# Performance work log

Hardware: AMD Instinct MI355X
Metric: run time of the kernel (lower is better)

Reference implementation:

```python
import jax, jax.numpy as jnp
import numpy as np

B, D_CAT, C_IN, C_OUT, K, H, W = 16, 512, 256, 256, 3, 64, 64


def setup_inputs() -> dict:
    key = jax.random.key(0)
    ks = jax.random.split(key, 9)
    inp = {
        "x": jax.random.normal(ks[0], (B, C_IN, H, W), dtype=jnp.float32),
        "y": jax.random.normal(ks[1], (B, D_CAT), dtype=jnp.float32),
        # EqualLinear stack: d_catin -> in_channels, then n_dl=2 layers in_channels -> in_channels
        "w0": jax.random.normal(ks[2], (C_IN, D_CAT), dtype=jnp.float32) / np.sqrt(D_CAT),
        "b0": jnp.zeros((C_IN,), dtype=jnp.float32),
        "w1": jax.random.normal(ks[3], (C_IN, C_IN), dtype=jnp.float32) / np.sqrt(C_IN),
        "b1": jnp.zeros((C_IN,), dtype=jnp.float32),
        "w2": jax.random.normal(ks[4], (C_IN, C_IN), dtype=jnp.float32) / np.sqrt(C_IN),
        "b2": jnp.zeros((C_IN,), dtype=jnp.float32),
        # shared conv weight (O, I, k, k), modulated per sample
        "conv_w": jax.random.normal(ks[5], (C_OUT, C_IN, K, K), dtype=jnp.float32) / np.sqrt(C_IN * K * K),
    }
    return inp


def _lrelu(z):
    # nn.LeakyReLU default negative_slope = 0.01
    return jnp.where(z >= 0, z, 0.01 * z)


def reference(x, y, w0, b0, w1, b1, w2, b2, conv_w):
    # style MLP (EqualLinear stack with LeakyReLU)
    s = _lrelu(y @ w0.T + b0)          # (B, C_in)
    s = _lrelu(s @ w1.T + b1)
    s = _lrelu(s @ w2.T + b2)
    # Per-sample weight modulation: conv(x[b], W * s[b, None, :, None, None]).
    # Since the scale is per input channel (no demodulation), this is exactly
    # equivalent to scaling the input channels and running one shared conv —
    # the fused form a custom kernel would use.
    x_mod = x * s[:, :, None, None]    # (B, C_in, H, W)
    out = jax.lax.conv_general_dilated(
        x_mod, conv_w,
        window_strides=(1, 1),
        padding=((1, 1), (1, 1)),
        dimension_numbers=("NCHW", "OIHW", "NCHW"),
    )  # (B, C_out, H, W); conv has bias=False in _DyConv
    return out
```

## Files before the change

### kernel.cpp

```cpp
#include <hip/hip_runtime.h>

typedef short bf16x8 __attribute__((ext_vector_type(8)));
typedef float f32x4 __attribute__((ext_vector_type(4)));
typedef unsigned short ushort8 __attribute__((ext_vector_type(8)));
typedef unsigned short ushort4v __attribute__((ext_vector_type(4)));

#define BATCH 16
#define DCAT 512
#define CIN 256
#define COUT 256
#define HH 64
#define WW 64
#define HP 66
#define WP 66
#define PLANE (HP * WP * 8)

__device__ __forceinline__ unsigned short f2bf(float f) {
  unsigned int u = __float_as_uint(f);
  unsigned int r = (u + 0x7fffu + ((u >> 16) & 1u)) >> 16;
  return (unsigned short)r;
}

template <int IN_DIM>
__global__ void __launch_bounds__(256) mlp_layer(const float* __restrict__ in,
                                                 const float* __restrict__ w,
                                                 const float* __restrict__ bias,
                                                 float* __restrict__ out) {
  int wid = threadIdx.x >> 6, lane = threadIdx.x & 63;
  int oidx = blockIdx.x * 4 + wid;
  int b = oidx >> 8, c = oidx & 255;
  const float* wr = w + (size_t)c * IN_DIM;
  const float* ir = in + (size_t)b * IN_DIM;
  float sum = 0.f;
#pragma unroll
  for (int d0 = 0; d0 < IN_DIM; d0 += 256) {
    f32x4 wv = *(const f32x4*)(wr + d0 + lane * 4);
    f32x4 iv = *(const f32x4*)(ir + d0 + lane * 4);
    sum += wv[0] * iv[0] + wv[1] * iv[1] + wv[2] * iv[2] + wv[3] * iv[3];
  }
#pragma unroll
  for (int off = 32; off; off >>= 1) sum += __shfl_xor(sum, off, 64);
  if (lane == 0) {
    float a = sum + bias[c];
    out[oidx] = a >= 0.f ? a : 0.01f * a;
  }
}

__global__ void __launch_bounds__(256) prep_all(const float* __restrict__ t1,
                                                const float* __restrict__ w2,
                                                const float* __restrict__ b2,
                                                const float* __restrict__ x,
                                                const float* __restrict__ cw,
                                                unsigned short* __restrict__ xpad,
                                                unsigned short* __restrict__ wt) {
  int blk = blockIdx.x;
  int tid = threadIdx.x;

  if (blk >= 1024) {
    int idx = (blk - 1024) * 256 + tid;
    int t = idx / 16384;
    int r = idx - t * 16384;
    int o = r >> 6, i4 = r & 63;
    ushort4v v;
#pragma unroll
    for (int j = 0; j < 4; j++) v[j] = f2bf(cw[(o * 256 + i4 * 4 + j) * 9 + t]);
    *(ushort4v*)(wt + ((size_t)(t * COUT + o)) * CIN + i4 * 4) = v;
    return;
  }

  int h = blk & 1, c8 = (blk >> 1) & 31, b = blk >> 6;
  int wid = tid >> 6, lane = tid & 63;

  float tv = t1[b * CIN + tid];
  float pj[8];
#pragma unroll
  for (int j = 0; j < 8; j++) pj[j] = w2[(size_t)(c8 * 8 + j) * CIN + tid] * tv;

  const float* xb = x + ((size_t)(b * CIN + c8 * 8)) * (HH * WW);
  int gg0 = h * 512 + tid;
  int gg1 = gg0 + 256;
  int hh0 = (gg0 >> 4) + 1, w00 = (gg0 & 15) * 4 + 1;
  int hh1 = (gg1 >> 4) + 1, w01 = (gg1 & 15) * 4 + 1;
  int base0 = (hh0 - 1) * WW + (w00 - 1);
  int base1 = (hh1 - 1) * WW + (w01 - 1);
  f32x4 v0[8], v1[8];
#pragma unroll
  for (int j = 0; j < 8; j++) v0[j] = *(const f32x4*)(xb + j * (HH * WW) + base0);
#pragma unroll
  for (int j = 0; j < 8; j++) v1[j] = *(const f32x4*)(xb + j * (HH * WW) + base1);

#pragma unroll
  for (int off = 32; off; off >>= 1)
#pragma unroll
    for (int j = 0; j < 8; j++) pj[j] += __shfl_xor(pj[j], off, 64);
  __shared__ float red[4][8];
  __shared__ float sv_sh[8];
  if (lane == 0)
#pragma unroll
    for (int j = 0; j < 8; j++) red[wid][j] = pj[j];
  __syncthreads();
  if (tid < 8) {
    float a = red[0][tid] + red[1][tid] + red[2][tid] + red[3][tid] + b2[c8 * 8 + tid];
    sv_sh[tid] = a >= 0.f ? a : 0.01f * a;
  }
  __syncthreads();
  float sv[8];
#pragma unroll
  for (int j = 0; j < 8; j++) sv[j] = sv_sh[j];

  unsigned short* xp = xpad + ((size_t)(b * 32 + c8)) * PLANE;

  if (tid < 130) {
    int i = h * 130 + tid;
    int bh, bw;
    if (i < 66) { bh = 0; bw = i; }
    else if (i < 132) { bh = 65; bw = i - 66; }
    else if (i < 196) { bh = i - 132 + 1; bw = 0; }
    else { bh = i - 196 + 1; bw = 65; }
    ushort8 z = {0, 0, 0, 0, 0, 0, 0, 0};
    *(ushort8*)(xp + (bh * WP + bw) * 8) = z;
  }

  unsigned short* op0 = xp + (hh0 * WP + w00) * 8;
  unsigned short* op1 = xp + (hh1 * WP + w01) * 8;
#pragma unroll
  for (int t2 = 0; t2 < 4; t2++) {
    ushort8 o;
#pragma unroll
    for (int j = 0; j < 8; j++) o[j] = f2bf(v0[j][t2] * sv[j]);
    *(ushort8*)(op0 + t2 * 8) = o;
  }
#pragma unroll
  for (int t2 = 0; t2 < 4; t2++) {
    ushort8 o;
#pragma unroll
    for (int j = 0; j < 8; j++) o[j] = f2bf(v1[j][t2] * sv[j]);
    *(ushort8*)(op1 + t2 * 8) = o;
  }
}

__device__ __forceinline__ void gl2lds16(const void* g, void* l) {
  __builtin_amdgcn_global_load_lds((const __attribute__((address_space(1))) void*)g,
                                   (__attribute__((address_space(3))) void*)l, 16, 0, 0);
}

__global__ void __launch_bounds__(512, 4) gemm_conv(const unsigned short* __restrict__ xpad,
                                                    const unsigned short* __restrict__ wt,
                                                    float* __restrict__ out) {
  __shared__ unsigned short As[128 * 64];
  __shared__ unsigned short Bs[256 * 64];
  int tid = threadIdx.x;
  int wid = tid >> 6, lane = tid & 63;
  int bid = blockIdx.x;
  int m_t = (bid & 7) * 64 + (bid >> 3);
  int m0 = m_t << 7;
  int b = m0 >> 12;
  int h0 = (m0 >> 6) & 63;
  int wm = wid & 1, wn = wid >> 1;

  f32x4 acc[4][4];
#pragma unroll
  for (int mi = 0; mi < 4; mi++)
#pragma unroll
    for (int ni = 0; ni < 4; ni++) acc[mi][ni] = (f32x4){0.f, 0.f, 0.f, 0.f};

  int p = tid >> 3;
  int cs = tid & 7;
  int gsA = cs ^ (p & 7);
  const unsigned short* aL =
      xpad + ((size_t)((b * 32 + gsA) * HP + h0)) * (WP * 8) + p * 8;
  int o_l = tid >> 3;
  const unsigned short* bL = wt + o_l * CIN + (cs ^ (o_l & 7)) * 8;

  char* As_w0 = (char*)As + wid * 1024;
  char* As_w1 = (char*)As + 8192 + wid * 1024;
  char* Bs_w0 = (char*)Bs + wid * 1024;
  char* Bs_w1 = (char*)Bs + 8192 + wid * 1024;
  char* Bs_w2 = (char*)Bs + 16384 + wid * 1024;
  char* Bs_w3 = (char*)Bs + 24576 + wid * 1024;

  int rA = wm * 64 + (lane & 15);
  int rB = wn * 64 + (lane & 15);
  int qa = lane >> 4;
  int offA0 = rA * 128 + ((qa ^ (rA & 7)) * 16);
  int offA1 = rA * 128 + (((qa + 4) ^ (rA & 7)) * 16);
  int offB0 = rB * 128 + ((qa ^ (rB & 7)) * 16);
  int offB1 = rB * 128 + (((qa + 4) ^ (rB & 7)) * 16);

  for (int kh = 0; kh < 3; kh++) {
    for (int kw = 0; kw < 3; kw++) {
      const unsigned short* aT = aL + (kh * WP + kw) * 8;
      const unsigned short* bT = bL + (kh * 3 + kw) * (COUT * CIN);
#pragma unroll
      for (int kc2 = 0; kc2 < 4; kc2++) {
        const unsigned short* aG = aT + kc2 * (8 * PLANE);
        const unsigned short* bG = bT + kc2 * 64;
        gl2lds16(aG, As_w0);
        gl2lds16(aG + WP * 8, As_w1);
        gl2lds16(bG, Bs_w0);
        gl2lds16(bG + 64 * CIN, Bs_w1);
        gl2lds16(bG + 128 * CIN, Bs_w2);
        gl2lds16(bG + 192 * CIN, Bs_w3);
        __syncthreads();
#pragma unroll
        for (int kb = 0; kb < 2; kb++) {
          int oa = kb ? offA1 : offA0;
          int ob = kb ? offB1 : offB0;
          bf16x8 av[4], bv[4];
#pragma unroll
          for (int mi = 0; mi < 4; mi++)
            av[mi] = *(const bf16x8*)((const char*)As + oa + mi * 2048);
#pragma unroll
          for (int ni = 0; ni < 4; ni++)
            bv[ni] = *(const bf16x8*)((const char*)Bs + ob + ni * 2048);
#pragma unroll
          for (int mi = 0; mi < 4; mi++)
#pragma unroll
            for (int ni = 0; ni < 4; ni++)
              acc[mi][ni] = __builtin_amdgcn_mfma_f32_16x16x32_bf16(av[mi], bv[ni],
                                                                    acc[mi][ni], 0, 0, 0);
        }
        __syncthreads();
      }
    }
  }

  int pixbase = m0 & 4095;
  int quad = lane >> 4;
  int col = lane & 15;
#pragma unroll
  for (int mi = 0; mi < 4; mi++) {
    int pm = pixbase + wm * 64 + mi * 16 + quad * 4;
#pragma unroll
    for (int ni = 0; ni < 4; ni++) {
      int on = wn * 64 + ni * 16 + col;
      float* op = out + ((size_t)(b * COUT + on) << 12) + pm;
      *(f32x4*)op = acc[mi][ni];
    }
  }
}

extern "C" void kernel_launch(void* const* d_in, const int* in_sizes, int n_in,
                              void* d_out, int out_size, void* d_ws, size_t ws_size,
                              hipStream_t stream) {
  const float* x = (const float*)d_in[0];
  const float* y = (const float*)d_in[1];
  const float* w0 = (const float*)d_in[2];
  const float* b0 = (const float*)d_in[3];
  const float* w1 = (const float*)d_in[4];
  const float* b1 = (const float*)d_in[5];
  const float* w2 = (const float*)d_in[6];
  const float* b2 = (const float*)d_in[7];
  const float* cw = (const float*)d_in[8];
  float* out = (float*)d_out;

  char* ws = (char*)d_ws;
  float* t0 = (float*)ws;
  float* t1 = (float*)(ws + 16384);
  unsigned short* wt = (unsigned short*)(ws + 32768);
  unsigned short* xpad = (unsigned short*)(ws + 32768 + 9 * COUT * CIN * 2);

  mlp_layer<DCAT><<<BATCH * CIN / 4, 256, 0, stream>>>(y, w0, b0, t0);
  mlp_layer<CIN><<<BATCH * CIN / 4, 256, 0, stream>>>(t0, w1, b1, t1);
  prep_all<<<1024 + 576, 256, 0, stream>>>(t1, w2, b2, x, cw, xpad, wt);
  gemm_conv<<<BATCH * HH * WW / 128, 512, 0, stream>>>(xpad, wt, out);
}
```

Baseline: 210.6 us.

## Stage input halo once per channel chunk and double-buffer weights in conv GEMM

New measurement: 199.0 us. 5.5% less time.

```diff
diff --git a/kernel.cpp b/kernel.cpp
--- a/kernel.cpp
+++ b/kernel.cpp
@@ -14,6 +14,8 @@
 #define HP 66
 #define WP 66
 #define PLANE (HP * WP * 8)
+#define AHALO 52224
+#define BBUF 32768
 
 __device__ __forceinline__ unsigned short f2bf(float f) {
   unsigned int u = __float_as_uint(f);
@@ -144,83 +146,104 @@
                                    (__attribute__((address_space(3))) void*)l, 16, 0, 0);
 }
 
-__global__ void __launch_bounds__(512, 4) gemm_conv(const unsigned short* __restrict__ xpad,
+__global__ void __launch_bounds__(512, 1) gemm_conv(const unsigned short* __restrict__ xpad,
                                                     const unsigned short* __restrict__ wt,
                                                     float* __restrict__ out) {
-  __shared__ unsigned short As[128 * 64];
-  __shared__ unsigned short Bs[256 * 64];
+  __shared__ __align__(16) char lds[AHALO + 2 * BBUF];
   int tid = threadIdx.x;
   int wid = tid >> 6, lane = tid & 63;
   int bid = blockIdx.x;
-  int m_t = (bid & 7) * 64 + (bid >> 3);
-  int m0 = m_t << 7;
+  int m_t = (bid & 7) * 32 + (bid >> 3);
+  int m0 = m_t << 8;
   int b = m0 >> 12;
   int h0 = (m0 >> 6) & 63;
   int wm = wid & 1, wn = wid >> 1;
 
-  f32x4 acc[4][4];
-#pragma unroll
-  for (int mi = 0; mi < 4; mi++)
+  f32x4 acc[8][4];
+#pragma unroll
+  for (int mi = 0; mi < 8; mi++)
 #pragma unroll
     for (int ni = 0; ni < 4; ni++) acc[mi][ni] = (f32x4){0.f, 0.f, 0.f, 0.f};
 
-  int p = tid >> 3;
-  int cs = tid & 7;
-  int gsA = cs ^ (p & 7);
-  const unsigned short* aL =
-      xpad + ((size_t)((b * 32 + gsA) * HP + h0)) * (WP * 8) + p * 8;
+  const unsigned short* aSrc[7];
+#pragma unroll
+  for (int i = 0; i < 7; i++) {
+    int c = (i * 8 + wid) * 64 + lane;
+    int e = c >> 3, cs = c & 7;
+    int gs = cs ^ (e & 7);
+    int rh = e / 68, wc = e - rh * 68;
+    aSrc[i] = xpad + ((size_t)((b * 32 + gs) * HP + (h0 + rh))) * (WP * 8) + wc * 8;
+  }
+
   int o_l = tid >> 3;
-  const unsigned short* bL = wt + o_l * CIN + (cs ^ (o_l & 7)) * 8;
-
-  char* As_w0 = (char*)As + wid * 1024;
-  char* As_w1 = (char*)As + 8192 + wid * 1024;
-  char* Bs_w0 = (char*)Bs + wid * 1024;
-  char* Bs_w1 = (char*)Bs + 8192 + wid * 1024;
-  char* Bs_w2 = (char*)Bs + 16384 + wid * 1024;
-  char* Bs_w3 = (char*)Bs + 24576 + wid * 1024;
-
-  int rA = wm * 64 + (lane & 15);
-  int rB = wn * 64 + (lane & 15);
+  int csb = tid & 7;
+  const unsigned short* bL = wt + o_l * CIN + ((csb ^ (o_l & 7)) * 8);
+
   int qa = lane >> 4;
-  int offA0 = rA * 128 + ((qa ^ (rA & 7)) * 16);
-  int offA1 = rA * 128 + (((qa + 4) ^ (rA & 7)) * 16);
+  int l15 = lane & 15;
+  int rB = wn * 64 + l15;
   int offB0 = rB * 128 + ((qa ^ (rB & 7)) * 16);
   int offB1 = rB * 128 + (((qa + 4) ^ (rB & 7)) * 16);
 
-  for (int kh = 0; kh < 3; kh++) {
-    for (int kw = 0; kw < 3; kw++) {
-      const unsigned short* aT = aL + (kh * WP + kw) * 8;
-      const unsigned short* bT = bL + (kh * 3 + kw) * (COUT * CIN);
-#pragma unroll
-      for (int kc2 = 0; kc2 < 4; kc2++) {
-        const unsigned short* aG = aT + kc2 * (8 * PLANE);
-        const unsigned short* bG = bT + kc2 * 64;
-        gl2lds16(aG, As_w0);
-        gl2lds16(aG + WP * 8, As_w1);
-        gl2lds16(bG, Bs_w0);
-        gl2lds16(bG + 64 * CIN, Bs_w1);
-        gl2lds16(bG + 128 * CIN, Bs_w2);
-        gl2lds16(bG + 192 * CIN, Bs_w3);
-        __syncthreads();
+  int cur = 0;
+  for (int kc2 = 0; kc2 < 4; kc2++) {
+    size_t kofs = (size_t)kc2 * 8 * PLANE;
+#pragma unroll
+    for (int i = 0; i < 6; i++)
+      gl2lds16(aSrc[i] + kofs, lds + (i * 8 + wid) * 1024);
+    if (wid < 3) gl2lds16(aSrc[6] + kofs, lds + (48 + wid) * 1024);
+    {
+      const unsigned short* bG = bL + kc2 * 64;
+      char* dB = lds + AHALO + cur * BBUF + wid * 1024;
+#pragma unroll
+      for (int q = 0; q < 4; q++) gl2lds16(bG + q * 64 * CIN, dB + q * 8192);
+    }
+    __syncthreads();
+
+    for (int kh = 0; kh < 3; kh++) {
+      for (int kw = 0; kw < 3; kw++) {
+        int tap = kh * 3 + kw;
+        if (tap < 8) {
+          const unsigned short* bG = bL + (tap + 1) * (COUT * CIN) + kc2 * 64;
+          char* dB = lds + AHALO + (cur ^ 1) * BBUF + wid * 1024;
+#pragma unroll
+          for (int q = 0; q < 4; q++) gl2lds16(bG + q * 64 * CIN, dB + q * 8192);
+        }
+
+        int eb = (wm * 2 + kh) * 68 + l15 + kw;
+        int s0 = eb & 7, s1 = (eb + 4) & 7;
+        int a00 = eb * 128 + ((qa ^ s0) * 16);
+        int a01 = (eb + 68) * 128 + ((qa ^ s1) * 16);
+        int a10 = eb * 128 + (((qa + 4) ^ s0) * 16);
+        int a11 = (eb + 68) * 128 + (((qa + 4) ^ s1) * 16);
+        const char* Bb = lds + AHALO + cur * BBUF;
+
 #pragma unroll
         for (int kb = 0; kb < 2; kb++) {
-          int oa = kb ? offA1 : offA0;
+          int oa0 = kb ? a10 : a00;
+          int oa1 = kb ? a11 : a01;
           int ob = kb ? offB1 : offB0;
-          bf16x8 av[4], bv[4];
-#pragma unroll
-          for (int mi = 0; mi < 4; mi++)
-            av[mi] = *(const bf16x8*)((const char*)As + oa + mi * 2048);
+          bf16x8 av[8], bv[4];
+#pragma unroll
+          for (int mi = 0; mi < 4; mi++) {
+            av[mi] = *(const bf16x8*)(lds + oa0 + mi * 2048);
+            av[4 + mi] = *(const bf16x8*)(lds + oa1 + mi * 2048);
+          }
 #pragma unroll
           for (int ni = 0; ni < 4; ni++)
-            bv[ni] = *(const bf16x8*)((const char*)Bs + ob + ni * 2048);
-#pragma unroll
-          for (int mi = 0; mi < 4; mi++)
+            bv[ni] = *(const bf16x8*)(Bb + ob + ni * 2048);
+          __builtin_amdgcn_s_setprio(1);
+#pragma unroll
+          for (int mi = 0; mi < 8; mi++)
 #pragma unroll
             for (int ni = 0; ni < 4; ni++)
               acc[mi][ni] = __builtin_amdgcn_mfma_f32_16x16x32_bf16(av[mi], bv[ni],
                                                                     acc[mi][ni], 0, 0, 0);
+          __builtin_amdgcn_s_setprio(0);
         }
+
         __syncthreads();
+        cur ^= 1;
       }
     }
   }
@@ -229,8 +252,8 @@
   int quad = lane >> 4;
   int col = lane & 15;
 #pragma unroll
-  for (int mi = 0; mi < 4; mi++) {
-    int pm = pixbase + wm * 64 + mi * 16 + quad * 4;
+  for (int mi = 0; mi < 8; mi++) {
+    int pm = pixbase + wm * 128 + mi * 16 + quad * 4;
 #pragma unroll
     for (int ni = 0; ni < 4; ni++) {
       int on = wn * 64 + ni * 16 + col;
@@ -255,13 +278,13 @@
   float* out = (float*)d_out;
 
   char* ws = (char*)d_ws;
-  float* t0 = (float*)ws;
-  float* t1 = (float*)(ws + 16384);
-  unsigned short* wt = (unsigned short*)(ws + 32768);
-  unsigned short* xpad = (unsigned short*)(ws + 32768 + 9 * COUT * CIN * 2);
+  unsigned short* xpad = (unsigned short*)ws;
+  unsigned short* wt = (unsigned short*)(ws + 35684352);
+  float* t0 = (float*)(ws + 35684352 + 2359296);
+  float* t1 = (float*)(ws + 35684352 + 2359296 + 16384);
 
   mlp_layer<DCAT><<<BATCH * CIN / 4, 256, 0, stream>>>(y, w0, b0, t0);
   mlp_layer<CIN><<<BATCH * CIN / 4, 256, 0, stream>>>(t0, w1, b1, t1);
   prep_all<<<1024 + 576, 256, 0, stream>>>(t1, w2, b2, x, cw, xpad, wt);
-  gemm_conv<<<BATCH * HH * WW / 128, 512, 0, stream>>>(xpad, wt, out);
-}
+  gemm_conv<<<BATCH * HH * WW / 256, 512, 0, stream>>>(xpad, wt, out);
+}
```
